# Performance work log

Measured on AMD Instinct MI355X. Metric: run time of the kernel, lower is better.

The kernel has to match this reference:

```python
import jax, jax.numpy as jnp
import numpy as np

N_HEAD = 16
D_HEAD = 64
D_MODEL = 1024
B, T = 2, 2048


def setup_inputs() -> dict:
    key = jax.random.key(0)
    ks = jax.random.split(key, 5)
    s = 1.0 / np.sqrt(D_MODEL)
    return {
        "x": jax.random.normal(ks[0], (B, T, D_MODEL), dtype=jnp.float32),
        "wq": jax.random.normal(ks[1], (D_MODEL, D_MODEL), dtype=jnp.float32) * s,
        "wk": jax.random.normal(ks[2], (D_MODEL, D_MODEL), dtype=jnp.float32) * s,
        "wv": jax.random.normal(ks[3], (D_MODEL, D_MODEL), dtype=jnp.float32) * s,
        "wo": jax.random.normal(ks[4], (D_MODEL, D_MODEL), dtype=jnp.float32) * s,
    }


def reference(x, wq, wk, wv, wo):
    Bb, Tt, D = x.shape
    H, Dh = N_HEAD, D_HEAD
    # Linear projections (flax Linear: y = x @ kernel), split heads
    q = (x @ wq).reshape(Bb, Tt, H, Dh)
    k = (x @ wk).reshape(Bb, Tt, H, Dh)
    v = (x @ wv).reshape(Bb, Tt, H, Dh)
    scale = jnp.sqrt(jnp.asarray(Dh)).astype(x.dtype)
    scores = jnp.einsum('bthd,bshd->bhts', q, k) / scale  # [B,H,T,T]
    mask = jnp.tril(jnp.ones((Tt, Tt), dtype=jnp.bool_))
    scores = jnp.where(mask, scores, jnp.finfo(scores.dtype).min)
    attn = jax.nn.softmax(scores, axis=-1)
    out = jnp.einsum('bhts,bshd->bthd', attn, v).reshape(Bb, Tt, D)
    return out @ wo
```

## Files before the change

kernel.cpp:

```cpp
#include <hip/hip_runtime.h>
#include <math.h>

#define DEV static __device__ __forceinline__

typedef __attribute__((ext_vector_type(4))) float f32x4;
typedef __attribute__((ext_vector_type(2))) unsigned u32x2;
typedef __attribute__((ext_vector_type(8))) __bf16 bf16x8;
typedef __attribute__((ext_vector_type(8))) unsigned short u16x8;
typedef __attribute__((ext_vector_type(4))) unsigned short u16x4;

constexpr int TB = 2;
constexpr int TT = 2048;
constexpr int DM = 1024;
constexpr int NH = 16;
constexpr int DH = 64;
constexpr int MR = TB * TT;
constexpr int SQKV = 3 * DM;

DEV unsigned short f2bf(float f) {
  union { float f; unsigned u; } v; v.f = f;
  return (unsigned short)((v.u + 0x7FFFu + ((v.u >> 16) & 1u)) >> 16);
}

DEV unsigned cvtpk(float a, float b) {
  unsigned r;
  asm("v_cvt_pk_bf16_f32 %0, %1, %2" : "=v"(r) : "v"(a), "v"(b));
  return r;
}

DEV void gld16(const void* g, void* l) {
  __builtin_amdgcn_global_load_lds((const __attribute__((address_space(1))) void*)g,
                                   (__attribute__((address_space(3))) void*)l, 16, 0, 0);
}

DEV bf16x8 ldsb8(const unsigned short* p) { return *(const bf16x8*)p; }

__global__ __launch_bounds__(256) void k_prep(const float* __restrict__ x,
                                              const float* __restrict__ w0,
                                              const float* __restrict__ w1,
                                              const float* __restrict__ w2,
                                              const float* __restrict__ w3,
                                              unsigned short* __restrict__ xb,
                                              unsigned short* __restrict__ wtdst) {
  __shared__ float tile[32][33];
  const int id = blockIdx.x, tid = threadIdx.x;
  if (id < 4096) {
    const int z = id >> 10, tl = id & 1023;
    const float* w = z == 0 ? w0 : z == 1 ? w1 : z == 2 ? w2 : w3;
    unsigned short* wt = wtdst + (size_t)z * DM * DM;
    const int n0 = (tl & 31) * 32, k0 = (tl >> 5) * 32;
    const int tx = tid & 31, ty = tid >> 5;
#pragma unroll
    for (int yy = 0; yy < 32; yy += 8)
      tile[ty + yy][tx] = w[(size_t)(k0 + ty + yy) * DM + n0 + tx];
    __syncthreads();
#pragma unroll
    for (int yy = 0; yy < 32; yy += 8)
      wt[(size_t)(n0 + ty + yy) * DM + k0 + tx] = f2bf(tile[tx][ty + yy]);
  } else {
    const int i = ((id - 4096) * 256 + tid) * 8;
    f32x4 a = *(const f32x4*)(x + i);
    f32x4 b = *(const f32x4*)(x + i + 4);
    u16x8 o;
#pragma unroll
    for (int j = 0; j < 4; ++j) { o[j] = f2bf(a[j]); o[j + 4] = f2bf(b[j]); }
    *(u16x8*)(xb + i) = o;
  }
}

DEV void store_c(float* p, float v) { *p = v; }
DEV void store_c(unsigned short* p, float v) { *p = f2bf(v); }

__global__ __launch_bounds__(512) void k_gemm_qkv(const unsigned short* __restrict__ A,
                                                  const unsigned short* __restrict__ Bt,
                                                  unsigned short* __restrict__ C,
                                                  float ascale,
                                                  unsigned short* __restrict__ vt) {
  constexpr int K = DM, N = SQKV;
  __shared__ alignas(16) unsigned short As[128 * 32];
  __shared__ alignas(16) unsigned short Bs[128 * 32];
  const int tid = threadIdx.x;
  const int m0 = blockIdx.y * 128, n0 = blockIdx.x * 128;
  const int lane = tid & 63, w = tid >> 6;
  const int lr = lane & 15, lg = lane >> 4;
  const int wm = w >> 2, wn = w & 3;
  const int srow = tid >> 2, scc = (tid & 3) ^ ((srow >> 1) & 3);
  const unsigned short* Ab = A + (size_t)(m0 + srow) * K + scc * 8;
  const unsigned short* Bb = Bt + (size_t)(n0 + srow) * K + scc * 8;
  f32x4 acc[4][2] = {};
  for (int k0 = 0; k0 < K; k0 += 32) {
    gld16(Ab + k0, (void*)(As + tid * 8));
    gld16(Bb + k0, (void*)(Bs + tid * 8));
    __syncthreads();
    bf16x8 af[4], bfr[2];
#pragma unroll
    for (int i = 0; i < 4; ++i) {
      const int row = wm * 64 + i * 16 + lr;
      af[i] = ldsb8(As + row * 32 + ((lg ^ ((row >> 1) & 3)) * 8));
    }
#pragma unroll
    for (int j = 0; j < 2; ++j) {
      const int row = wn * 32 + j * 16 + lr;
      bfr[j] = ldsb8(Bs + row * 32 + ((lg ^ ((row >> 1) & 3)) * 8));
    }
#pragma unroll
    for (int i = 0; i < 4; ++i)
#pragma unroll
      for (int j = 0; j < 2; ++j)
        acc[i][j] = __builtin_amdgcn_mfma_f32_16x16x32_bf16(af[i], bfr[j], acc[i][j], 0, 0, 0);
    __syncthreads();
  }
#pragma unroll
  for (int i = 0; i < 4; ++i)
#pragma unroll
    for (int j = 0; j < 2; ++j) {
      const int row = m0 + wm * 64 + i * 16 + lg * 4;
      const int col = n0 + wn * 32 + j * 16 + lr;
      if (col >= 2 * DM) {
        const int hh = (col - 2 * DM) >> 6, dd = (col - 2 * DM) & 63;
        const int bb = row >> 11, sg = row & (TT - 1);
        const int t = sg >> 6, sl = sg & 63;
        const int g = ((sl >> 5) << 2) | ((sl >> 2) & 3);
        const int half = (sl >> 4) & 1;
        const int cch = g ^ (dd & 7);
        u16x4 pk;
#pragma unroll
        for (int r = 0; r < 4; ++r) pk[r] = f2bf(acc[i][j][r]);
        *(u16x4*)(vt + (size_t)((bb * NH + hh) * 32 + t) * 4096 + dd * 64 + cch * 8 + half * 4) = pk;
      } else {
        const float s = (col < DM) ? ascale : 1.0f;
#pragma unroll
        for (int r = 0; r < 4; ++r)
          store_c(C + (size_t)(row + r) * N + col, acc[i][j][r] * s);
      }
    }
}

__global__ __launch_bounds__(512) void k_gemm_out(const unsigned short* __restrict__ A,
                                                  const unsigned short* __restrict__ Bt,
                                                  float* __restrict__ C) {
  constexpr int K = DM, N = DM;
  __shared__ alignas(16) unsigned short As[128 * 32];
  __shared__ alignas(16) unsigned short Bs[64 * 32];
  const int tid = threadIdx.x;
  const int m0 = blockIdx.y * 128, n0 = blockIdx.x * 64;
  const int lane = tid & 63, w = tid >> 6;
  const int lr = lane & 15, lg = lane >> 4;
  const int wm = w >> 1, wn = w & 1;
  const int srow = tid >> 2, scc = (tid & 3) ^ ((srow >> 1) & 3);
  const unsigned short* Ab = A + (size_t)(m0 + srow) * K + scc * 8;
  const unsigned short* Bb = (tid < 256) ? Bt + (size_t)(n0 + srow) * K + scc * 8 : nullptr;
  f32x4 acc[2][2] = {};
  for (int k0 = 0; k0 < K; k0 += 32) {
    gld16(Ab + k0, (void*)(As + tid * 8));
    if (tid < 256) gld16(Bb + k0, (void*)(Bs + tid * 8));
    __syncthreads();
    bf16x8 af[2], bfr[2];
#pragma unroll
    for (int i = 0; i < 2; ++i) {
      const int row = wm * 32 + i * 16 + lr;
      af[i] = ldsb8(As + row * 32 + ((lg ^ ((row >> 1) & 3)) * 8));
    }
#pragma unroll
    for (int j = 0; j < 2; ++j) {
      const int row = wn * 32 + j * 16 + lr;
      bfr[j] = ldsb8(Bs + row * 32 + ((lg ^ ((row >> 1) & 3)) * 8));
    }
#pragma unroll
    for (int i = 0; i < 2; ++i)
#pragma unroll
      for (int j = 0; j < 2; ++j)
        acc[i][j] = __builtin_amdgcn_mfma_f32_16x16x32_bf16(af[i], bfr[j], acc[i][j], 0, 0, 0);
    __syncthreads();
  }
#pragma unroll
  for (int i = 0; i < 2; ++i)
#pragma unroll
    for (int j = 0; j < 2; ++j) {
      const int row = m0 + wm * 32 + i * 16 + lg * 4;
      const int col = n0 + wn * 32 + j * 16 + lr;
#pragma unroll
      for (int r = 0; r < 4; ++r) C[(size_t)(row + r) * N + col] = acc[i][j][r];
    }
}

__global__ __launch_bounds__(512) void k_attn9(const unsigned short* __restrict__ QKV,
                                               const unsigned short* __restrict__ Vt,
                                               unsigned short* __restrict__ O) {
  __shared__ alignas(16) unsigned short Ks[3][64 * 64];
  __shared__ alignas(16) unsigned short Vs[3][64 * 64];
  const int id = blockIdx.x;
  const int pairIdx = id & 255;
  const int bh = pairIdx >> 3, pi = pairIdx & 7;
  const int j = (id < 256) ? pi : 15 - pi;
  const int b = bh >> 4, h = bh & 15;
  const int q0 = j * 128;
  const int tid = threadIdx.x, lane = tid & 63, w = tid >> 6;
  const int lr = lane & 15, lg = lane >> 4;
  const int lsw = lr & 7;
  const int qw = q0 + w * 16;
  const unsigned short* Qg = QKV + (size_t)b * TT * SQKV + h * DH;
  const unsigned short* Kg = QKV + (size_t)b * TT * SQKV + DM + h * DH;
  const unsigned short* Vg = Vt + (size_t)bh * 32 * 4096;

  bf16x8 qf[2];
#pragma unroll
  for (int c2 = 0; c2 < 2; ++c2)
    qf[c2] = *(const bf16x8*)(Qg + (size_t)(qw + lr) * SQKV + c2 * 32 + lg * 8);

  f32x4 acco[4] = {};
  float mrun = -1e30f, lrun = 0.f;

  const int krow = tid >> 3, kcc = (tid & 7) ^ (krow & 7);
  const unsigned short* kbase = Kg + (size_t)krow * SQKV + kcc * 8;
  const unsigned short* vbase = Vg + tid * 8;
  auto stage = [&](int buf, int t) {
    gld16(kbase + (size_t)t * 64 * SQKV, (void*)(Ks[buf] + tid * 8));
    gld16(vbase + (size_t)t * 4096, (void*)(Vs[buf] + tid * 8));
  };

  const int nt = 2 * j + 2;
  stage(0, 0);
  stage(1, 1);
  int buf = 0;
  for (int t = 0; t < nt; ++t) {
    if (t + 1 < nt) {
      asm volatile("s_waitcnt vmcnt(2)" ::: "memory");
    } else {
      asm volatile("s_waitcnt vmcnt(0)" ::: "memory");
    }
    __builtin_amdgcn_s_barrier();
    if (t + 2 < nt) {
      int nb = buf + 2; if (nb >= 3) nb -= 3;
      stage(nb, t + 2);
    }
    const int s0 = t * 64;
    if (s0 <= qw + 15) {
      const unsigned short* Kb_ = Ks[buf];
      const unsigned short* Vb_ = Vs[buf];
      f32x4 st[4] = {};
      __builtin_amdgcn_s_setprio(1);
#pragma unroll
      for (int ct = 0; ct < 4; ++ct)
#pragma unroll
        for (int c2 = 0; c2 < 2; ++c2) {
          bf16x8 kf = ldsb8(Kb_ + (ct * 16 + lr) * 64 + (((c2 * 4 + lg) ^ lsw) * 8));
          st[ct] = __builtin_amdgcn_mfma_f32_16x16x32_bf16(kf, qf[c2], st[ct], 0, 0, 0);
        }
      __builtin_amdgcn_s_setprio(0);
      float p[4][4];
      const bool diag = (s0 + 63 >= qw);
      const int qrel = qw + lr - s0;
      if (diag) {
#pragma unroll
        for (int ct = 0; ct < 4; ++ct)
#pragma unroll
          for (int r = 0; r < 4; ++r) {
            float v = st[ct][r];
            if (ct * 16 + lg * 4 + r > qrel) v = -1e30f;
            p[ct][r] = v;
          }
      } else {
#pragma unroll
        for (int ct = 0; ct < 4; ++ct)
#pragma unroll
          for (int r = 0; r < 4; ++r) p[ct][r] = st[ct][r];
      }
      float m0_ = fmaxf(fmaxf(p[0][0], p[0][1]), p[0][2]);
      float m1_ = fmaxf(fmaxf(p[0][3], p[1][0]), p[1][1]);
      float m2_ = fmaxf(fmaxf(p[1][2], p[1][3]), p[2][0]);
      float m3_ = fmaxf(fmaxf(p[2][1], p[2][2]), p[2][3]);
      float m4_ = fmaxf(fmaxf(p[3][0], p[3][1]), p[3][2]);
      float mx = fmaxf(fmaxf(fmaxf(m0_, m1_), fmaxf(m2_, m3_)), fmaxf(m4_, p[3][3]));
      mx = fmaxf(mx, __shfl_xor(mx, 16));
      mx = fmaxf(mx, __shfl_xor(mx, 32));
      if (!__all(mx <= mrun + 11.5f)) {
        const float mn = fmaxf(mrun, mx);
        const float aa = __builtin_exp2f(mrun - mn);
        mrun = mn;
        lrun *= aa;
        float aab[4];
#pragma unroll
        for (int r = 0; r < 4; ++r) aab[r] = __shfl(aa, lg * 4 + r);
#pragma unroll
        for (int dt = 0; dt < 4; ++dt)
#pragma unroll
          for (int r = 0; r < 4; ++r) acco[dt][r] *= aab[r];
      }
      f32x4 rs4 = {0.f, 0.f, 0.f, 0.f};
#pragma unroll
      for (int ct = 0; ct < 4; ++ct)
#pragma unroll
        for (int r = 0; r < 4; ++r) {
          p[ct][r] = __builtin_exp2f(p[ct][r] - mrun);
          rs4[r] += p[ct][r];
        }
      float rs = (rs4[0] + rs4[1]) + (rs4[2] + rs4[3]);
      rs += __shfl_xor(rs, 16);
      rs += __shfl_xor(rs, 32);
      lrun += rs;
      bf16x8 pf[2];
#pragma unroll
      for (int ks = 0; ks < 2; ++ks) {
        union { unsigned w4[4]; bf16x8 v; } pu;
        pu.w4[0] = cvtpk(p[2 * ks][0], p[2 * ks][1]);
        pu.w4[1] = cvtpk(p[2 * ks][2], p[2 * ks][3]);
        pu.w4[2] = cvtpk(p[2 * ks + 1][0], p[2 * ks + 1][1]);
        pu.w4[3] = cvtpk(p[2 * ks + 1][2], p[2 * ks + 1][3]);
        pf[ks] = pu.v;
      }
      __builtin_amdgcn_s_setprio(1);
#pragma unroll
      for (int dt = 0; dt < 4; ++dt) {
        const unsigned short* Vrow = Vb_ + (dt * 16 + lr) * 64;
#pragma unroll
        for (int ks = 0; ks < 2; ++ks) {
          bf16x8 vf = ldsb8(Vrow + (((ks * 4 + lg) ^ lsw) * 8));
          acco[dt] = __builtin_amdgcn_mfma_f32_16x16x32_bf16(pf[ks], vf, acco[dt], 0, 0, 0);
        }
      }
      __builtin_amdgcn_s_setprio(0);
    }
    if (++buf >= 3) buf = 0;
  }
  const float linv = 1.f / lrun;
  float lb[4];
#pragma unroll
  for (int r = 0; r < 4; ++r) lb[r] = __shfl(linv, lg * 4 + r);
#pragma unroll
  for (int dt = 0; dt < 4; ++dt)
#pragma unroll
    for (int r = 0; r < 4; ++r) {
      const int q = qw + lg * 4 + r;
      O[(size_t)(b * TT + q) * DM + h * DH + dt * 16 + lr] = f2bf(acco[dt][r] * lb[r]);
    }
}

extern "C" void kernel_launch(void* const* d_in, const int* in_sizes, int n_in,
                              void* d_out, int out_size, void* d_ws, size_t ws_size,
                              hipStream_t stream) {
  const float* x = (const float*)d_in[0];
  const float* wq = (const float*)d_in[1];
  const float* wk = (const float*)d_in[2];
  const float* wv = (const float*)d_in[3];
  const float* wo = (const float*)d_in[4];
  float* out = (float*)d_out;
  char* ws = (char*)d_ws;
  const size_t MB = 1u << 20;
  unsigned short* xb = (unsigned short*)(ws);
  unsigned short* wqt = (unsigned short*)(ws + 8 * MB);
  unsigned short* wot = (unsigned short*)(ws + 14 * MB);
  unsigned short* QKVb = (unsigned short*)(ws + 16 * MB);
  unsigned short* Vtb = (unsigned short*)(ws + 40 * MB);

  k_prep<<<dim3(6144), 256, 0, stream>>>(x, wq, wk, wv, wo, xb, wqt);
  k_gemm_qkv<<<dim3(24, 32), 512, 0, stream>>>(xb, wqt, QKVb, 0.18033688f, Vtb);
  k_attn9<<<dim3(512), 512, 0, stream>>>(QKVb, Vtb, xb);
  k_gemm_out<<<dim3(16, 32), 512, 0, stream>>>(xb, wot, out);
}
```

Before: 119.3 us.

## Process two query sub-tiles per wave in attention, halving block size

```diff
diff --git a/kernel.cpp b/kernel.cpp
--- a/kernel.cpp
+++ b/kernel.cpp
@@ -184,9 +184,9 @@
     }
 }
 
-__global__ __launch_bounds__(512) void k_attn9(const unsigned short* __restrict__ QKV,
-                                               const unsigned short* __restrict__ Vt,
-                                               unsigned short* __restrict__ O) {
+__global__ __launch_bounds__(256) void k_attn10(const unsigned short* __restrict__ QKV,
+                                                const unsigned short* __restrict__ Vt,
+                                                unsigned short* __restrict__ O) {
   __shared__ alignas(16) unsigned short Ks[3][64 * 64];
   __shared__ alignas(16) unsigned short Vs[3][64 * 64];
   const int id = blockIdx.x;
@@ -198,25 +198,30 @@
   const int tid = threadIdx.x, lane = tid & 63, w = tid >> 6;
   const int lr = lane & 15, lg = lane >> 4;
   const int lsw = lr & 7;
-  const int qw = q0 + w * 16;
+  const int qw = q0 + w * 32;
   const unsigned short* Qg = QKV + (size_t)b * TT * SQKV + h * DH;
   const unsigned short* Kg = QKV + (size_t)b * TT * SQKV + DM + h * DH;
   const unsigned short* Vg = Vt + (size_t)bh * 32 * 4096;
 
-  bf16x8 qf[2];
-#pragma unroll
-  for (int c2 = 0; c2 < 2; ++c2)
-    qf[c2] = *(const bf16x8*)(Qg + (size_t)(qw + lr) * SQKV + c2 * 32 + lg * 8);
-
-  f32x4 acco[4] = {};
-  float mrun = -1e30f, lrun = 0.f;
-
-  const int krow = tid >> 3, kcc = (tid & 7) ^ (krow & 7);
-  const unsigned short* kbase = Kg + (size_t)krow * SQKV + kcc * 8;
+  bf16x8 qf[2][2];
+#pragma unroll
+  for (int qi = 0; qi < 2; ++qi)
+#pragma unroll
+    for (int c2 = 0; c2 < 2; ++c2)
+      qf[qi][c2] = *(const bf16x8*)(Qg + (size_t)(qw + qi * 16 + lr) * SQKV + c2 * 32 + lg * 8);
+
+  f32x4 acco[2][4] = {};
+  float mrun[2] = {-1e30f, -1e30f}, lrun[2] = {0.f, 0.f};
+
+  const int kcc = (tid & 7);
+  const unsigned short* kb0 = Kg + (size_t)(tid >> 3) * SQKV + (kcc ^ ((tid >> 3) & 7)) * 8;
+  const unsigned short* kb1 = Kg + (size_t)((tid + 256) >> 3) * SQKV + (kcc ^ (((tid + 256) >> 3) & 7)) * 8;
   const unsigned short* vbase = Vg + tid * 8;
   auto stage = [&](int buf, int t) {
-    gld16(kbase + (size_t)t * 64 * SQKV, (void*)(Ks[buf] + tid * 8));
+    gld16(kb0 + (size_t)t * 64 * SQKV, (void*)(Ks[buf] + tid * 8));
+    gld16(kb1 + (size_t)t * 64 * SQKV, (void*)(Ks[buf] + (tid + 256) * 8));
     gld16(vbase + (size_t)t * 4096, (void*)(Vs[buf] + tid * 8));
+    gld16(vbase + (size_t)t * 4096 + 2048, (void*)(Vs[buf] + (tid + 256) * 8));
   };
 
   const int nt = 2 * j + 2;
@@ -225,7 +230,7 @@
   int buf = 0;
   for (int t = 0; t < nt; ++t) {
     if (t + 1 < nt) {
-      asm volatile("s_waitcnt vmcnt(2)" ::: "memory");
+      asm volatile("s_waitcnt vmcnt(4)" ::: "memory");
     } else {
       asm volatile("s_waitcnt vmcnt(0)" ::: "memory");
     }
@@ -235,80 +240,92 @@
       stage(nb, t + 2);
     }
     const int s0 = t * 64;
-    if (s0 <= qw + 15) {
+    if (s0 <= qw + 31) {
       const unsigned short* Kb_ = Ks[buf];
       const unsigned short* Vb_ = Vs[buf];
-      f32x4 st[4] = {};
+      f32x4 st[2][4] = {};
       __builtin_amdgcn_s_setprio(1);
 #pragma unroll
       for (int ct = 0; ct < 4; ++ct)
 #pragma unroll
         for (int c2 = 0; c2 < 2; ++c2) {
           bf16x8 kf = ldsb8(Kb_ + (ct * 16 + lr) * 64 + (((c2 * 4 + lg) ^ lsw) * 8));
-          st[ct] = __builtin_amdgcn_mfma_f32_16x16x32_bf16(kf, qf[c2], st[ct], 0, 0, 0);
+#pragma unroll
+          for (int qi = 0; qi < 2; ++qi)
+            st[qi][ct] = __builtin_amdgcn_mfma_f32_16x16x32_bf16(kf, qf[qi][c2], st[qi][ct], 0, 0, 0);
         }
       __builtin_amdgcn_s_setprio(0);
-      float p[4][4];
-      const bool diag = (s0 + 63 >= qw);
-      const int qrel = qw + lr - s0;
-      if (diag) {
+      bf16x8 pf[2][2];
+      float aa[2];
+      bool resc[2];
+#pragma unroll
+      for (int qi = 0; qi < 2; ++qi) {
+        float p[4][4];
+        const int qg = qw + qi * 16;
+        const int qrel = qg + lr - s0;
+        if (s0 + 63 >= qg) {
+#pragma unroll
+          for (int ct = 0; ct < 4; ++ct)
+#pragma unroll
+            for (int r = 0; r < 4; ++r) {
+              float v = st[qi][ct][r];
+              if (ct * 16 + lg * 4 + r > qrel) v = -1e30f;
+              p[ct][r] = v;
+            }
+        } else {
+#pragma unroll
+          for (int ct = 0; ct < 4; ++ct)
+#pragma unroll
+            for (int r = 0; r < 4; ++r) p[ct][r] = st[qi][ct][r];
+        }
+        float m0_ = fmaxf(fmaxf(p[0][0], p[0][1]), p[0][2]);
+        float m1_ = fmaxf(fmaxf(p[0][3], p[1][0]), p[1][1]);
+        float m2_ = fmaxf(fmaxf(p[1][2], p[1][3]), p[2][0]);
+        float m3_ = fmaxf(fmaxf(p[2][1], p[2][2]), p[2][3]);
+        float m4_ = fmaxf(fmaxf(p[3][0], p[3][1]), p[3][2]);
+        float mx = fmaxf(fmaxf(fmaxf(m0_, m1_), fmaxf(m2_, m3_)), fmaxf(m4_, p[3][3]));
+        mx = fmaxf(mx, __shfl_xor(mx, 16));
+        mx = fmaxf(mx, __shfl_xor(mx, 32));
+        resc[qi] = !__all(mx <= mrun[qi] + 11.5f);
+        if (resc[qi]) {
+          const float mn = fmaxf(mrun[qi], mx);
+          aa[qi] = __builtin_exp2f(mrun[qi] - mn);
+          mrun[qi] = mn;
+          lrun[qi] *= aa[qi];
+        }
+        f32x4 rs4 = {0.f, 0.f, 0.f, 0.f};
 #pragma unroll
         for (int ct = 0; ct < 4; ++ct)
 #pragma unroll
           for (int r = 0; r < 4; ++r) {
-            float v = st[ct][r];
-            if (ct * 16 + lg * 4 + r > qrel) v = -1e30f;
-            p[ct][r] = v;
+            p[ct][r] = __builtin_exp2f(p[ct][r] - mrun[qi]);
+            rs4[r] += p[ct][r];
           }
-      } else {
-#pragma unroll
-        for (int ct = 0; ct < 4; ++ct)
-#pragma unroll
-          for (int r = 0; r < 4; ++r) p[ct][r] = st[ct][r];
+        float rs = (rs4[0] + rs4[1]) + (rs4[2] + rs4[3]);
+        rs += __shfl_xor(rs, 16);
+        rs += __shfl_xor(rs, 32);
+        lrun[qi] += rs;
+#pragma unroll
+        for (int ks = 0; ks < 2; ++ks) {
+          union { unsigned w4[4]; bf16x8 v; } pu;
+          pu.w4[0] = cvtpk(p[2 * ks][0], p[2 * ks][1]);
+          pu.w4[1] = cvtpk(p[2 * ks][2], p[2 * ks][3]);
+          pu.w4[2] = cvtpk(p[2 * ks + 1][0], p[2 * ks + 1][1]);
+          pu.w4[3] = cvtpk(p[2 * ks + 1][2], p[2 * ks + 1][3]);
+          pf[qi][ks] = pu.v;
+        }
       }
-      float m0_ = fmaxf(fmaxf(p[0][0], p[0][1]), p[0][2]);
-      float m1_ = fmaxf(fmaxf(p[0][3], p[1][0]), p[1][1]);
-      float m2_ = fmaxf(fmaxf(p[1][2], p[1][3]), p[2][0]);
-      float m3_ = fmaxf(fmaxf(p[2][1], p[2][2]), p[2][3]);
-      float m4_ = fmaxf(fmaxf(p[3][0], p[3][1]), p[3][2]);
-      float mx = fmaxf(fmaxf(fmaxf(m0_, m1_), fmaxf(m2_, m3_)), fmaxf(m4_, p[3][3]));
-      mx = fmaxf(mx, __shfl_xor(mx, 16));
-      mx = fmaxf(mx, __shfl_xor(mx, 32));
-      if (!__all(mx <= mrun + 11.5f)) {
-        const float mn = fmaxf(mrun, mx);
-        const float aa = __builtin_exp2f(mrun - mn);
-        mrun = mn;
-        lrun *= aa;
-        float aab[4];
-#pragma unroll
-        for (int r = 0; r < 4; ++r) aab[r] = __shfl(aa, lg * 4 + r);
-#pragma unroll
-        for (int dt = 0; dt < 4; ++dt)
-#pragma unroll
-          for (int r = 0; r < 4; ++r) acco[dt][r] *= aab[r];
-      }
-      f32x4 rs4 = {0.f, 0.f, 0.f, 0.f};
-#pragma unroll
-      for (int ct = 0; ct < 4; ++ct)
-#pragma unroll
-        for (int r = 0; r < 4; ++r) {
-          p[ct][r] = __builtin_exp2f(p[ct][r] - mrun);
-          rs4[r] += p[ct][r];
-        }
-      float rs = (rs4[0] + rs4[1]) + (rs4[2] + rs4[3]);
-      rs += __shfl_xor(rs, 16);
-      rs += __shfl_xor(rs, 32);
-      lrun += rs;
-      bf16x8 pf[2];
-#pragma unroll
-      for (int ks = 0; ks < 2; ++ks) {
-        union { unsigned w4[4]; bf16x8 v; } pu;
-        pu.w4[0] = cvtpk(p[2 * ks][0], p[2 * ks][1]);
-        pu.w4[1] = cvtpk(p[2 * ks][2], p[2 * ks][3]);
-        pu.w4[2] = cvtpk(p[2 * ks + 1][0], p[2 * ks + 1][1]);
-        pu.w4[3] = cvtpk(p[2 * ks + 1][2], p[2 * ks + 1][3]);
-        pf[ks] = pu.v;
-      }
+#pragma unroll
+      for (int qi = 0; qi < 2; ++qi)
+        if (resc[qi]) {
+          float aab[4];
+#pragma unroll
+          for (int r = 0; r < 4; ++r) aab[r] = __shfl(aa[qi], lg * 4 + r);
+#pragma unroll
+          for (int dt = 0; dt < 4; ++dt)
+#pragma unroll
+            for (int r = 0; r < 4; ++r) acco[qi][dt][r] *= aab[r];
+        }
       __builtin_amdgcn_s_setprio(1);
 #pragma unroll
       for (int dt = 0; dt < 4; ++dt) {
@@ -316,24 +333,29 @@
 #pragma unroll
         for (int ks = 0; ks < 2; ++ks) {
           bf16x8 vf = ldsb8(Vrow + (((ks * 4 + lg) ^ lsw) * 8));
-          acco[dt] = __builtin_amdgcn_mfma_f32_16x16x32_bf16(pf[ks], vf, acco[dt], 0, 0, 0);
+#pragma unroll
+          for (int qi = 0; qi < 2; ++qi)
+            acco[qi][dt] = __builtin_amdgcn_mfma_f32_16x16x32_bf16(pf[qi][ks], vf, acco[qi][dt], 0, 0, 0);
         }
       }
       __builtin_amdgcn_s_setprio(0);
     }
     if (++buf >= 3) buf = 0;
   }
-  const float linv = 1.f / lrun;
-  float lb[4];
-#pragma unroll
-  for (int r = 0; r < 4; ++r) lb[r] = __shfl(linv, lg * 4 + r);
-#pragma unroll
-  for (int dt = 0; dt < 4; ++dt)
-#pragma unroll
-    for (int r = 0; r < 4; ++r) {
-      const int q = qw + lg * 4 + r;
-      O[(size_t)(b * TT + q) * DM + h * DH + dt * 16 + lr] = f2bf(acco[dt][r] * lb[r]);
-    }
+#pragma unroll
+  for (int qi = 0; qi < 2; ++qi) {
+    const float linv = 1.f / lrun[qi];
+    float lb[4];
+#pragma unroll
+    for (int r = 0; r < 4; ++r) lb[r] = __shfl(linv, lg * 4 + r);
+#pragma unroll
+    for (int dt = 0; dt < 4; ++dt)
+#pragma unroll
+      for (int r = 0; r < 4; ++r) {
+        const int q = qw + qi * 16 + lg * 4 + r;
+        O[(size_t)(b * TT + q) * DM + h * DH + dt * 16 + lr] = f2bf(acco[qi][dt][r] * lb[r]);
+      }
+  }
 }
 
 extern "C" void kernel_launch(void* const* d_in, const int* in_sizes, int n_in,
@@ -355,6 +377,6 @@
 
   k_prep<<<dim3(6144), 256, 0, stream>>>(x, wq, wk, wv, wo, xb, wqt);
   k_gemm_qkv<<<dim3(24, 32), 512, 0, stream>>>(xb, wqt, QKVb, 0.18033688f, Vtb);
-  k_attn9<<<dim3(512), 512, 0, stream>>>(QKVb, Vtb, xb);
+  k_attn10<<<dim3(512), 256, 0, stream>>>(QKVb, Vtb, xb);
   k_gemm_out<<<dim3(16, 32), 512, 0, stream>>>(xb, wot, out);
 }
```

Measured after the change: 135.4 us. 1.14x slower.

## Software-pipeline QK^T one tile ahead and deepen K/V ring to four buffers

Applied to the files above, without the earlier changes.

```diff
diff --git a/kernel.cpp b/kernel.cpp
--- a/kernel.cpp
+++ b/kernel.cpp
@@ -184,11 +184,11 @@
     }
 }
 
-__global__ __launch_bounds__(512) void k_attn9(const unsigned short* __restrict__ QKV,
-                                               const unsigned short* __restrict__ Vt,
-                                               unsigned short* __restrict__ O) {
-  __shared__ alignas(16) unsigned short Ks[3][64 * 64];
-  __shared__ alignas(16) unsigned short Vs[3][64 * 64];
+__global__ __launch_bounds__(512) void k_attn11(const unsigned short* __restrict__ QKV,
+                                                const unsigned short* __restrict__ Vt,
+                                                unsigned short* __restrict__ O) {
+  __shared__ alignas(16) unsigned short Ks[4][64 * 64];
+  __shared__ alignas(16) unsigned short Vs[4][64 * 64];
   const int id = blockIdx.x;
   const int pairIdx = id & 255;
   const int bh = pairIdx >> 3, pi = pairIdx & 7;
@@ -218,45 +218,60 @@
     gld16(kbase + (size_t)t * 64 * SQKV, (void*)(Ks[buf] + tid * 8));
     gld16(vbase + (size_t)t * 4096, (void*)(Vs[buf] + tid * 8));
   };
+  auto qkt = [&](const unsigned short* Kb_, f32x4* st) {
+#pragma unroll
+    for (int ct = 0; ct < 4; ++ct) {
+      st[ct] = f32x4{0.f, 0.f, 0.f, 0.f};
+#pragma unroll
+      for (int c2 = 0; c2 < 2; ++c2) {
+        bf16x8 kf = ldsb8(Kb_ + (ct * 16 + lr) * 64 + (((c2 * 4 + lg) ^ lsw) * 8));
+        st[ct] = __builtin_amdgcn_mfma_f32_16x16x32_bf16(kf, qf[c2], st[ct], 0, 0, 0);
+      }
+    }
+  };
 
   const int nt = 2 * j + 2;
   stage(0, 0);
   stage(1, 1);
-  int buf = 0;
+  if (nt > 2) {
+    stage(2, 2);
+    asm volatile("s_waitcnt vmcnt(2)" ::: "memory");
+  } else {
+    asm volatile("s_waitcnt vmcnt(0)" ::: "memory");
+  }
+  __builtin_amdgcn_s_barrier();
+
+  f32x4 stc[4];
+  qkt(Ks[0], stc);
+
   for (int t = 0; t < nt; ++t) {
-    if (t + 1 < nt) {
-      asm volatile("s_waitcnt vmcnt(2)" ::: "memory");
-    } else {
-      asm volatile("s_waitcnt vmcnt(0)" ::: "memory");
-    }
-    __builtin_amdgcn_s_barrier();
-    if (t + 2 < nt) {
-      int nb = buf + 2; if (nb >= 3) nb -= 3;
-      stage(nb, t + 2);
+    if (t > 0) {
+      if (t + 2 < nt) {
+        asm volatile("s_waitcnt vmcnt(2)" ::: "memory");
+      } else {
+        asm volatile("s_waitcnt vmcnt(0)" ::: "memory");
+      }
+      __builtin_amdgcn_s_barrier();
+    }
+    if (t + 3 < nt) stage((t + 3) & 3, t + 3);
+    f32x4 stn[4];
+    const bool dn = (t + 1 < nt) && ((t + 1) * 64 <= qw + 15);
+    if (dn) {
+      __builtin_amdgcn_s_setprio(1);
+      qkt(Ks[(t + 1) & 3], stn);
+      __builtin_amdgcn_s_setprio(0);
     }
     const int s0 = t * 64;
     if (s0 <= qw + 15) {
-      const unsigned short* Kb_ = Ks[buf];
-      const unsigned short* Vb_ = Vs[buf];
-      f32x4 st[4] = {};
-      __builtin_amdgcn_s_setprio(1);
-#pragma unroll
-      for (int ct = 0; ct < 4; ++ct)
-#pragma unroll
-        for (int c2 = 0; c2 < 2; ++c2) {
-          bf16x8 kf = ldsb8(Kb_ + (ct * 16 + lr) * 64 + (((c2 * 4 + lg) ^ lsw) * 8));
-          st[ct] = __builtin_amdgcn_mfma_f32_16x16x32_bf16(kf, qf[c2], st[ct], 0, 0, 0);
-        }
-      __builtin_amdgcn_s_setprio(0);
+      const unsigned short* Vb_ = Vs[t & 3];
       float p[4][4];
-      const bool diag = (s0 + 63 >= qw);
       const int qrel = qw + lr - s0;
-      if (diag) {
+      if (s0 + 63 >= qw) {
 #pragma unroll
         for (int ct = 0; ct < 4; ++ct)
 #pragma unroll
           for (int r = 0; r < 4; ++r) {
-            float v = st[ct][r];
+            float v = stc[ct][r];
             if (ct * 16 + lg * 4 + r > qrel) v = -1e30f;
             p[ct][r] = v;
           }
@@ -264,7 +279,7 @@
 #pragma unroll
         for (int ct = 0; ct < 4; ++ct)
 #pragma unroll
-          for (int r = 0; r < 4; ++r) p[ct][r] = st[ct][r];
+          for (int r = 0; r < 4; ++r) p[ct][r] = stc[ct][r];
       }
       float m0_ = fmaxf(fmaxf(p[0][0], p[0][1]), p[0][2]);
       float m1_ = fmaxf(fmaxf(p[0][3], p[1][0]), p[1][1]);
@@ -321,7 +336,9 @@
       }
       __builtin_amdgcn_s_setprio(0);
     }
-    if (++buf >= 3) buf = 0;
+    if (dn) {
+      stc[0] = stn[0]; stc[1] = stn[1]; stc[2] = stn[2]; stc[3] = stn[3];
+    }
   }
   const float linv = 1.f / lrun;
   float lb[4];
@@ -355,6 +372,6 @@
 
   k_prep<<<dim3(6144), 256, 0, stream>>>(x, wq, wk, wv, wo, xb, wqt);
   k_gemm_qkv<<<dim3(24, 32), 512, 0, stream>>>(xb, wqt, QKVb, 0.18033688f, Vtb);
-  k_attn9<<<dim3(512), 512, 0, stream>>>(QKVb, Vtb, xb);
+  k_attn11<<<dim3(512), 512, 0, stream>>>(QKVb, Vtb, xb);
   k_gemm_out<<<dim3(16, 32), 512, 0, stream>>>(xb, wot, out);
 }
```

Measured after the change: 122.0 us. +2.3%, slower.
